# Kernel optimization log

Hardware: AMD Instinct MI355X
Metric: run time of the kernel (lower is better)

Reference implementation:

```python
import jax, jax.numpy as jnp
import numpy as np
from jax import lax

B, C, H, W = 4, 64, 240, 320
K = 15   # filter_size
R = 3    # kernel_size
EPS = 1e-5
SLOPE = 0.2  # assumed LeakyReLU slope in convbnlrelu


def _bn(x, gamma, beta, mean, var):
    # inference-mode batchnorm folded into scale/shift
    inv = gamma / jnp.sqrt(var + EPS)
    return x * inv[None, :, None, None] + (beta - mean * inv)[None, :, None, None]


def _conv(x, w, pad):
    return lax.conv_general_dilated(x, w, (1, 1), [(pad, pad), (pad, pad)],
                                    dimension_numbers=('NCHW', 'OIHW', 'NCHW'))


def setup_inputs() -> dict:
    key = jax.random.key(0)
    ks = jax.random.split(key, 12)
    f32 = jnp.float32
    return dict(
        depth=jax.random.normal(ks[0], (B, 1, H, W), f32),
        feature=jax.random.normal(ks[1], (B, C, H, W), f32),
        w1=jax.random.normal(ks[2], (C, 1, 1, 1), f32) * 0.5,
        g1=jnp.ones((C,), f32), b1=jnp.zeros((C,), f32),
        m1=jax.random.normal(ks[3], (C,), f32) * 0.1,
        v1=jax.random.uniform(ks[4], (C,), f32, 0.5, 1.5),
        ww=jax.random.normal(ks[5], (R * R, 2 * C, 3, 3), f32) * 0.05,
        gw=jnp.ones((R * R,), f32), bw=jnp.zeros((R * R,), f32),
        mw=jax.random.normal(ks[6], (R * R,), f32) * 0.1,
        vw=jax.random.uniform(ks[7], (R * R,), f32, 0.5, 1.5),
        wo=jax.random.normal(ks[8], (2 * R * R, 2 * C, 3, 3), f32) * 0.02,
        go=jnp.ones((2 * R * R,), f32), bo=jnp.zeros((2 * R * R,), f32),
        mo=jax.random.normal(ks[9], (2 * R * R,), f32) * 0.1,
        vo=jax.random.uniform(ks[10], (2 * R * R,), f32, 0.5, 1.5),
    )


def reference(depth, feature, w1, g1, b1, m1, v1, ww, gw, bw, mw, vw, wo, go, bo, mo, vo):
    # depth-guided conv + bn + leaky relu
    df = _bn(_conv(depth, w1, 0), g1, b1, m1, v1)
    df = jnp.where(df >= 0, df, SLOPE * df)
    cat = jnp.concatenate([df, feature], axis=1)           # (B, 2C, H, W)
    weight = jax.nn.sigmoid(_bn(_conv(cat, ww, 1), gw, bw, mw, vw))  # (B, R^2, H, W)
    offset = _bn(_conv(cat, wo, 1), go, bo, mo, vo)                   # (B, 2R^2, H, W)

    # DKN_Interpolate (residual=True): zero-mean the per-tap weights
    weight = weight - jnp.mean(weight, axis=1, keepdims=True)

    N = B * H * W
    off = offset.transpose(0, 2, 3, 1).reshape(N, R, R, 2)   # (..., 0)=x, (..., 1)=y
    wgt = weight.transpose(0, 2, 3, 1).reshape(N, R * R)

    # unfold depth into KxK patch per output pixel (row-major ky,kx like F.unfold)
    patches = lax.conv_general_dilated_patches(depth, (K, K), (1, 1),
                                               [(K // 2, K // 2)] * 2)  # (B, K*K, H, W)
    patches = patches.transpose(0, 2, 3, 1).reshape(N, K * K)

    vals = jnp.linspace(K // 2, K // 2 + R - 1, R).astype(depth.dtype)
    gx, gy = jnp.meshgrid(vals, vals, indexing='ij')
    grid = jnp.stack([gx, gy], axis=-1)                      # (R, R, 2)
    coord = (grid[None] + off) / K * 2.0 - 1.0               # normalized coords

    # grid_sample(align_corners=True, padding_mode='zeros') bilinear on KxK patch
    ix = (coord[..., 0] + 1.0) * 0.5 * (K - 1)               # x -> width index
    iy = (coord[..., 1] + 1.0) * 0.5 * (K - 1)               # y -> height index
    x0 = jnp.floor(ix)
    y0 = jnp.floor(iy)
    wx1 = ix - x0
    wy1 = iy - y0

    def gather(xf, yf):
        valid = (xf >= 0) & (xf <= K - 1) & (yf >= 0) & (yf <= K - 1)
        xi = jnp.clip(xf, 0, K - 1).astype(jnp.int32)
        yi = jnp.clip(yf, 0, K - 1).astype(jnp.int32)
        idx = (yi * K + xi).reshape(N, R * R)
        v = jnp.take_along_axis(patches, idx, axis=1).reshape(N, R, R)
        return jnp.where(valid, v, 0.0)

    samp = (gather(x0, y0) * (1 - wx1) * (1 - wy1)
            + gather(x0 + 1, y0) * wx1 * (1 - wy1)
            + gather(x0, y0 + 1) * (1 - wx1) * wy1
            + gather(x0 + 1, y0 + 1) * wx1 * wy1)            # (N, R, R)

    out = jnp.sum(samp.reshape(N, R * R) * wgt, axis=1).reshape(B, 1, H, W)
    return out + depth
```

## Files before the change

kernel.cpp:

```cpp
#include <hip/hip_runtime.h>
#include <hip/hip_bf16.h>
#include <math.h>

namespace {
constexpr int Bn = 4, Cn = 64, Hn = 240, Wn = 320;
constexpr int HW = Hn * Wn;
constexpr int Npix = Bn * HW;
constexpr float EPS = 1e-5f;
constexpr float SLOPE = 0.2f;
constexpr int TM = 16, TN = 16;
constexpr int HR = TM + 2, HC = TN + 2;
constexpr int NPXT = HR * HC;
constexpr int NGR = NPXT * 4;
constexpr int PHB = 1344 * 16;
constexpr int WROWS = 31, WCOLS = 31;
constexpr size_t BMAT_BYTES = 4 * 9 * 2 * 64 * 8 * 2;
constexpr size_t CONST_BYTES = 1024;
constexpr size_t PLANE_BYTES = (size_t)Bn * HW * 32 * 2;
constexpr size_t LO_OFF = BMAT_BYTES + CONST_BYTES;
constexpr size_t HI_OFF = LO_OFF + PLANE_BYTES;
constexpr size_t WS_NEED = HI_OFF + PLANE_BYTES;
}

typedef __attribute__((ext_vector_type(8))) short bf16x8;
typedef __attribute__((ext_vector_type(4))) float f32x4;

__device__ inline unsigned cvtpk(float lo, float hi) {
    unsigned r;
    asm("v_cvt_pk_bf16_f32 %0, %1, %2" : "=v"(r) : "v"(lo), "v"(hi));
    return r;
}

__device__ inline float fastexp(float x) {
    float e;
    asm("v_exp_f32 %0, %1" : "=v"(e) : "v"(x * 1.44269504f));
    return e;
}

__device__ inline float fastrcp(float x) {
    float r;
    asm("v_rcp_f32 %0, %1" : "=v"(r) : "v"(x));
    return r;
}

__device__ inline unsigned short f2bf(float f) {
    unsigned u = __builtin_bit_cast(unsigned, f);
    return (unsigned short)((u + 0x7fffu + ((u >> 16) & 1u)) >> 16);
}

__global__ __launch_bounds__(256) void prep_B(
    const float* __restrict__ ww, const float* __restrict__ wo,
    const float* __restrict__ w1, const float* __restrict__ g1,
    const float* __restrict__ b1, const float* __restrict__ m1,
    const float* __restrict__ v1,
    const float* __restrict__ gw, const float* __restrict__ bw,
    const float* __restrict__ mw, const float* __restrict__ vw,
    const float* __restrict__ go, const float* __restrict__ bo,
    const float* __restrict__ mo, const float* __restrict__ vo,
    unsigned short* __restrict__ Bf, float* __restrict__ cst)
{
    if (blockIdx.x == 18) {
        const int i = threadIdx.x;
        if (i < 64) {
            const float inv = g1[i] * rsqrtf(v1[i] + EPS);
            cst[i] = w1[i] * inv;
            cst[64 + i] = b1[i] - m1[i] * inv;
        } else if (i < 64 + 27) {
            const int j = i - 64;
            float g, bb, m, v;
            if (j < 9) { g = gw[j]; bb = bw[j]; m = mw[j]; v = vw[j]; }
            else       { g = go[j - 9]; bb = bo[j - 9]; m = mo[j - 9]; v = vo[j - 9]; }
            const float inv = g * rsqrtf(v + EPS);
            cst[128 + j] = inv;
            cst[155 + j] = bb - m * inv;
        }
        return;
    }
    const int f = blockIdx.x * 256 + threadIdx.x;
    if (f >= 4608) return;
    const int lane = f & 63, rest = f >> 6;
    const int n = rest & 1, tp = rest >> 1;
    const int t = tp % 9, p = tp / 9;
    const int col = n * 16 + (lane & 15);
    const int hi = lane >> 4;
    unsigned short o[8];
    #pragma unroll
    for (int j = 0; j < 8; ++j) {
        const int c = p * 32 + hi * 8 + j;
        float v = 0.0f;
        if (col < 9)       v = ww[((size_t)col * 128 + c) * 9 + t];
        else if (col < 27) v = wo[((size_t)(col - 9) * 128 + c) * 9 + t];
        o[j] = f2bf(v);
    }
    uint4 u;
    u.x = (unsigned)o[0] | ((unsigned)o[1] << 16);
    u.y = (unsigned)o[2] | ((unsigned)o[3] << 16);
    u.z = (unsigned)o[4] | ((unsigned)o[5] << 16);
    u.w = (unsigned)o[6] | ((unsigned)o[7] << 16);
    *(uint4*)(Bf + (size_t)f * 8) = u;
}

__global__ __launch_bounds__(512) void prep_F(
    const float* __restrict__ feature,
    unsigned short* __restrict__ lo, unsigned short* __restrict__ hi)
{
    const int y = blockIdx.x;
    const int b = blockIdx.y;
    const int lane = threadIdx.x & 63;
    const int g = threadIdx.x >> 6;
    const int c0 = g * 8;
    unsigned short* __restrict__ plane = (g < 4) ? lo : hi;
    const int slotg = g & 3;
    const float* __restrict__ fb = feature + (size_t)b * Cn * HW + (size_t)y * Wn;
    #pragma unroll
    for (int s = 0; s < 5; ++s) {
        const int x = s * 64 + lane;
        float v[8];
        #pragma unroll
        for (int j = 0; j < 8; ++j)
            v[j] = fb[(size_t)(c0 + j) * HW + x];
        uint4 u;
        u.x = cvtpk(v[0], v[1]); u.y = cvtpk(v[2], v[3]);
        u.z = cvtpk(v[4], v[5]); u.w = cvtpk(v[6], v[7]);
        const int slot = (slotg + ((x + 1) >> 1)) & 3;
        *(uint4*)(plane + (size_t)(b * HW + y * Wn + x) * 32 + slot * 8) = u;
    }
}

__global__ __launch_bounds__(256, 3) void dkn_main(
    const unsigned short* __restrict__ Bf,
    const float* __restrict__ cst,
    const unsigned short* __restrict__ catLo,
    const unsigned short* __restrict__ catHi,
    const float* __restrict__ depth,
    float* __restrict__ out)
{
    __shared__ __align__(16) char lds[2 * PHB];

    const int tid = threadIdx.x;
    const int lane = tid & 63, wv = tid >> 6;
    const int b = blockIdx.z;
    const int h0 = blockIdx.y * TM;
    const int w0 = blockIdx.x * TN;
    const float* __restrict__ dimg = depth + (size_t)b * HW;
    const float* __restrict__ dfA = cst;
    const float* __restrict__ dfB = cst + 64;
    const float* __restrict__ eInv = cst + 128;
    const float* __restrict__ eBias = cst + 155;

    char* buf0 = lds;
    char* buf1 = lds + PHB;
    float* winp = (float*)lds;
    float* ldsT = (float*)(lds + 3968);

    const bool interior = (blockIdx.y >= 1) && (blockIdx.y <= 13)
                       && (blockIdx.x >= 1) && (blockIdx.x <= 18);

    const int gdf = tid & 3;
    const int pxq = tid >> 2;
    auto stage_df = [&](int pt, char* buf) {
        const int c0 = pt * 32 + gdf * 8;
        const float4 A0 = *(const float4*)(dfA + c0);
        const float4 A1 = *(const float4*)(dfA + c0 + 4);
        const float4 B0 = *(const float4*)(dfB + c0);
        const float4 B1 = *(const float4*)(dfB + c0 + 4);
        const float Ac[8] = {A0.x, A0.y, A0.z, A0.w, A1.x, A1.y, A1.z, A1.w};
        const float Bc[8] = {B0.x, B0.y, B0.z, B0.w, B1.x, B1.y, B1.z, B1.w};
        #pragma unroll
        for (int s = 0; s < 6; ++s) {
            const int px = s * 64 + pxq;
            if (px < NPXT) {
                const int r = (px * 57) >> 10;
                const int lc = px - r * 18;
                const int y = h0 + r - 1, x = w0 + lc - 1;
                const bool ok = ((unsigned)y < (unsigned)Hn) && ((unsigned)x < (unsigned)Wn);
                const float d = ok ? dimg[y * Wn + x] : 0.0f;
                float v[8];
                #pragma unroll
                for (int j = 0; j < 8; ++j) {
                    float u = fmaf(Ac[j], d, Bc[j]);
                    u = fmaxf(u, SLOPE * u);
                    v[j] = ok ? u : 0.0f;
                }
                uint4 u4;
                u4.x = cvtpk(v[0], v[1]); u4.y = cvtpk(v[2], v[3]);
                u4.z = cvtpk(v[4], v[5]); u4.w = cvtpk(v[6], v[7]);
                const int slot = (gdf + (lc >> 1)) & 3;
                *(uint4*)(buf + px * 64 + slot * 16) = u4;
            }
        }
    };

    auto issue_gll = [&](const unsigned short* __restrict__ plane, char* buf) {
        #pragma unroll
        for (int s = 0; s < 6; ++s) {
            const int base = s * 256 + wv * 64;
            if (base < NGR) {
                int i = base + lane;
                i = min(i, NGR - 1);
                const int px = i >> 2, slot = i & 3;
                const int r = (px * 57) >> 10;
                const int lc = px - r * 18;
                const int y = min(max(h0 + r - 1, 0), Hn - 1);
                const int x = min(max(w0 + lc - 1, 0), Wn - 1);
                const unsigned short* src =
                    plane + (size_t)(b * HW + y * Wn + x) * 32 + slot * 8;
                __builtin_amdgcn_global_load_lds(
                    (const __attribute__((address_space(1))) void*)src,
                    (__attribute__((address_space(3))) void*)(buf + (size_t)base * 16),
                    16, 0, 0);
            }
        }
    };
    auto borderfix = [&](char* buf) {
        #pragma unroll
        for (int s = 0; s < 6; ++s) {
            const int i = s * 256 + tid;
            if (i < NGR) {
                const int px = i >> 2;
                const int r = (px * 57) >> 10;
                const int lc = px - r * 18;
                const int y = h0 + r - 1, x = w0 + lc - 1;
                if (((unsigned)y >= (unsigned)Hn) || ((unsigned)x >= (unsigned)Wn)) {
                    uint4 z = {0u, 0u, 0u, 0u};
                    *(uint4*)(buf + (size_t)i * 16) = z;
                }
            }
        }
    };

    const int l15 = lane & 15, hi16 = lane >> 4;
    f32x4 acc[4][2] = {};

    auto mfma_phase = [&](int p, const char* buf) {
        const unsigned short* Bp = Bf + (size_t)p * 9216;
        auto lda = [&](int row, int dx) -> bf16x8 {
            const int col = l15 + dx;
            const int slot = (hi16 + (col >> 1)) & 3;
            return *(const bf16x8*)(buf + (row * HC + col) * 64 + slot * 16);
        };
        auto ldb = [&](int idx) -> bf16x8 {
            return *(const bf16x8*)(Bp + ((size_t)idx * 64 + lane) * 8);
        };
        auto do_dy = [&](const bf16x8* A0, const bf16x8* A1,
                         const bf16x8* A2, const bf16x8* A3, const bf16x8* bb) {
            #pragma unroll
            for (int dx = 0; dx < 3; ++dx) {
                acc[0][0] = __builtin_amdgcn_mfma_f32_16x16x32_bf16(A0[dx], bb[dx*2+0], acc[0][0], 0, 0, 0);
                acc[0][1] = __builtin_amdgcn_mfma_f32_16x16x32_bf16(A0[dx], bb[dx*2+1], acc[0][1], 0, 0, 0);
                acc[1][0] = __builtin_amdgcn_mfma_f32_16x16x32_bf16(A1[dx], bb[dx*2+0], acc[1][0], 0, 0, 0);
                acc[1][1] = __builtin_amdgcn_mfma_f32_16x16x32_bf16(A1[dx], bb[dx*2+1], acc[1][1], 0, 0, 0);
                acc[2][0] = __builtin_amdgcn_mfma_f32_16x16x32_bf16(A2[dx], bb[dx*2+0], acc[2][0], 0, 0, 0);
                acc[2][1] = __builtin_amdgcn_mfma_f32_16x16x32_bf16(A2[dx], bb[dx*2+1], acc[2][1], 0, 0, 0);
                acc[3][0] = __builtin_amdgcn_mfma_f32_16x16x32_bf16(A3[dx], bb[dx*2+0], acc[3][0], 0, 0, 0);
                acc[3][1] = __builtin_amdgcn_mfma_f32_16x16x32_bf16(A3[dx], bb[dx*2+1], acc[3][1], 0, 0, 0);
            }
        };
        const int r0 = 4 * wv;
        bf16x8 a0[3], a1[3], a2[3], a3[3], a4[3], a5[3];
        bf16x8 b0[6], b1[6], b2[6];
        #pragma unroll
        for (int dx = 0; dx < 3; ++dx) {
            a0[dx] = lda(r0 + 0, dx);
            a1[dx] = lda(r0 + 1, dx);
            a2[dx] = lda(r0 + 2, dx);
            a3[dx] = lda(r0 + 3, dx);
        }
        #pragma unroll
        for (int i = 0; i < 6; ++i) b0[i] = ldb(i);
        #pragma unroll
        for (int dx = 0; dx < 3; ++dx) a4[dx] = lda(r0 + 4, dx);
        #pragma unroll
        for (int i = 0; i < 6; ++i) b1[i] = ldb(6 + i);
        do_dy(a0, a1, a2, a3, b0);
        #pragma unroll
        for (int dx = 0; dx < 3; ++dx) a5[dx] = lda(r0 + 5, dx);
        #pragma unroll
        for (int i = 0; i < 6; ++i) b2[i] = ldb(12 + i);
        do_dy(a1, a2, a3, a4, b1);
        do_dy(a2, a3, a4, a5, b2);
    };

    stage_df(0, buf0);
    __syncthreads();

    mfma_phase(0, buf0);
    stage_df(1, buf1);
    __syncthreads();

    issue_gll(catLo, buf0);
    mfma_phase(1, buf1);
    asm volatile("s_waitcnt vmcnt(0)" ::: "memory");
    if (!interior) borderfix(buf0);
    __syncthreads();

    issue_gll(catHi, buf1);
    mfma_phase(2, buf0);
    asm volatile("s_waitcnt vmcnt(0)" ::: "memory");
    if (!interior) borderfix(buf1);
    __syncthreads();

    float wvv[4];
    int widx[4];
    bool wok[4];
    #pragma unroll
    for (int s = 0; s < 4; ++s) {
        const int i = s * 256 + tid;
        const int r = (i * 2115) >> 16;
        const int c = i - r * 31;
        const int y = h0 + r - 7, x = w0 + c - 7;
        const bool inw = (i < WROWS * WCOLS);
        const bool oki = inw && ((unsigned)y < (unsigned)Hn) && ((unsigned)x < (unsigned)Wn);
        widx[s] = i;
        wok[s] = inw;
        wvv[s] = oki ? dimg[y * Wn + x] : 0.0f;
    }
    mfma_phase(3, buf1);
    #pragma unroll
    for (int s = 0; s < 4; ++s)
        if (wok[s]) winp[widx[s]] = wvv[s];
    __syncthreads();

    #pragma unroll
    for (int m = 0; m < 4; ++m) {
        const int oy = 4 * wv + m;
        #pragma unroll
        for (int n = 0; n < 2; ++n) {
            #pragma unroll
            for (int r = 0; r < 4; ++r) {
                const int ox = hi16 * 4 + r;
                ldsT[(oy * TN + ox) * 33 + n * 16 + l15] = acc[m][n][r];
            }
        }
    }
    __syncthreads();

    {
        const int oyl = tid >> 4, oxl = tid & 15;
        const int h = h0 + oyl, w = w0 + oxl;
        const float* row = ldsT + (size_t)tid * 33;

        float wgt[9];
        float wsum = 0.0f;
        #pragma unroll
        for (int j = 0; j < 9; ++j) {
            const float x = fmaf(row[j], eInv[j], eBias[j]);
            const float e = fastexp(x);
            const float s = e * fastrcp(1.0f + e);
            wgt[j] = s;
            wsum += s;
        }
        const float wm = wsum * (1.0f / 9.0f);
        #pragma unroll
        for (int j = 0; j < 9; ++j) wgt[j] -= wm;

        float offv[18];
        #pragma unroll
        for (int j = 0; j < 18; ++j)
            offv[j] = fmaf(row[9 + j], eInv[9 + j], eBias[9 + j]);

        auto sampleW = [&](float xf, float yf) -> float {
            const bool vld = (xf >= 0.0f) & (xf <= 14.0f) & (yf >= 0.0f) & (yf <= 14.0f);
            const int xi = min(max((int)xf, 0), 14);
            const int yi = min(max((int)yf, 0), 14);
            const float v = winp[(oyl + yi) * WCOLS + (oxl + xi)];
            return vld ? v : 0.0f;
        };

        float res = 0.0f;
        #pragma unroll
        for (int i = 0; i < 3; ++i) {
            #pragma unroll
            for (int j = 0; j < 3; ++j) {
                const int t = i * 3 + j;
                const float ox = offv[2 * t + 0];
                const float oy = offv[2 * t + 1];
                const float ix = (7.0f + (float)i + ox) * (14.0f / 15.0f);
                const float iy = (7.0f + (float)j + oy) * (14.0f / 15.0f);
                const float x0 = floorf(ix), y0 = floorf(iy);
                const float wx1 = ix - x0, wy1 = iy - y0;
                const float wx0 = 1.0f - wx1, wy0 = 1.0f - wy1;
                const float s =
                      sampleW(x0,        y0       ) * wx0 * wy0
                    + sampleW(x0 + 1.0f, y0       ) * wx1 * wy0
                    + sampleW(x0,        y0 + 1.0f) * wx0 * wy1
                    + sampleW(x0 + 1.0f, y0 + 1.0f) * wx1 * wy1;
                res = fmaf(s, wgt[t], res);
            }
        }
        out[((size_t)b * Hn + h) * Wn + w] = res + winp[(oyl + 7) * WCOLS + (oxl + 7)];
    }
}

__global__ __launch_bounds__(256) void dkn_fused_f32(
    const float* __restrict__ depth, const float* __restrict__ feature,
    const float* __restrict__ w1, const float* __restrict__ g1,
    const float* __restrict__ b1, const float* __restrict__ m1,
    const float* __restrict__ v1, const float* __restrict__ ww,
    const float* __restrict__ gw, const float* __restrict__ bw,
    const float* __restrict__ mw, const float* __restrict__ vw,
    const float* __restrict__ wo, const float* __restrict__ go,
    const float* __restrict__ bo, const float* __restrict__ mo,
    const float* __restrict__ vo, float* __restrict__ out)
{
    const int n = blockIdx.x * blockDim.x + threadIdx.x;
    if (n >= Npix) return;
    const int w = n % Wn;
    const int h = (n / Wn) % Hn;
    const int b = n / (Wn * Hn);
    const float* __restrict__ dimg = depth + (size_t)b * HW;
    const float* __restrict__ fimg = feature + (size_t)b * Cn * HW;
    float d9[9], msk[9]; int off9[9];
    #pragma unroll
    for (int ky = 0; ky < 3; ++ky)
        #pragma unroll
        for (int kx = 0; kx < 3; ++kx) {
            const int t = ky * 3 + kx;
            const int y = h + ky - 1, x = w + kx - 1;
            const bool ok = ((unsigned)y < (unsigned)Hn) && ((unsigned)x < (unsigned)Wn);
            off9[t] = min(max(y, 0), Hn - 1) * Wn + min(max(x, 0), Wn - 1);
            d9[t] = dimg[off9[t]];
            msk[t] = ok ? 1.0f : 0.0f;
        }
    float accW[9], accO[18];
    #pragma unroll
    for (int o = 0; o < 9; ++o) accW[o] = 0.0f;
    #pragma unroll
    for (int o = 0; o < 18; ++o) accO[o] = 0.0f;
    for (int c = 0; c < Cn; ++c) {
        const float inv = g1[c] * rsqrtf(v1[c] + EPS);
        const float A = w1[c] * inv, Bc = b1[c] - m1[c] * inv;
        float v9[9];
        #pragma unroll
        for (int t = 0; t < 9; ++t) {
            const float x = fmaf(A, d9[t], Bc);
            v9[t] = msk[t] * fmaxf(x, SLOPE * x);
        }
        const float* wwc = ww + c * 9;
        const float* woc = wo + c * 9;
        #pragma unroll
        for (int o = 0; o < 9; ++o)
            #pragma unroll
            for (int t = 0; t < 9; ++t) accW[o] = fmaf(wwc[o * 1152 + t], v9[t], accW[o]);
        #pragma unroll
        for (int o = 0; o < 18; ++o)
            #pragma unroll
            for (int t = 0; t < 9; ++t) accO[o] = fmaf(woc[o * 1152 + t], v9[t], accO[o]);
    }
    for (int c = 0; c < Cn; ++c) {
        const float* fc = fimg + (size_t)c * HW;
        float v9[9];
        #pragma unroll
        for (int t = 0; t < 9; ++t) v9[t] = msk[t] * fc[off9[t]];
        const float* wwc = ww + (64 + c) * 9;
        const float* woc = wo + (64 + c) * 9;
        #pragma unroll
        for (int o = 0; o < 9; ++o)
            #pragma unroll
            for (int t = 0; t < 9; ++t) accW[o] = fmaf(wwc[o * 1152 + t], v9[t], accW[o]);
        #pragma unroll
        for (int o = 0; o < 18; ++o)
            #pragma unroll
            for (int t = 0; t < 9; ++t) accO[o] = fmaf(woc[o * 1152 + t], v9[t], accO[o]);
    }
    float wgt[9];
    float wsum = 0.0f;
    #pragma unroll
    for (int j = 0; j < 9; ++j) {
        const float inv = gw[j] * rsqrtf(vw[j] + EPS);
        const float x = fmaf(accW[j], inv, bw[j] - mw[j] * inv);
        const float s = 1.0f / (1.0f + expf(-x));
        wgt[j] = s; wsum += s;
    }
    const float wm = wsum * (1.0f / 9.0f);
    #pragma unroll
    for (int j = 0; j < 9; ++j) wgt[j] -= wm;
    float offv[18];
    #pragma unroll
    for (int j = 0; j < 18; ++j) {
        const float inv = go[j] * rsqrtf(vo[j] + EPS);
        offv[j] = fmaf(accO[j], inv, bo[j] - mo[j] * inv);
    }
    auto sampleD = [&](float xf, float yf) -> float {
        const bool vld = (xf >= 0.0f) & (xf <= 14.0f) & (yf >= 0.0f) & (yf <= 14.0f);
        const float xc = fminf(fmaxf(xf, 0.0f), 14.0f);
        const float yc = fminf(fmaxf(yf, 0.0f), 14.0f);
        const int xi = (int)xc, yi = (int)yc;
        const int yy = h + yi - 7, xx = w + xi - 7;
        const bool okimg = ((unsigned)yy < (unsigned)Hn) && ((unsigned)xx < (unsigned)Wn);
        return (vld && okimg) ? dimg[yy * Wn + xx] : 0.0f;
    };
    float res = 0.0f;
    #pragma unroll
    for (int i = 0; i < 3; ++i)
        #pragma unroll
        for (int j = 0; j < 3; ++j) {
            const int t = i * 3 + j;
            const float ox = offv[2 * t + 0], oy = offv[2 * t + 1];
            const float ix = (7.0f + (float)i + ox) * (14.0f / 15.0f);
            const float iy = (7.0f + (float)j + oy) * (14.0f / 15.0f);
            const float x0 = floorf(ix), y0 = floorf(iy);
            const float wx1 = ix - x0, wy1 = iy - y0;
            const float s = sampleD(x0, y0) * (1.0f - wx1) * (1.0f - wy1)
                          + sampleD(x0 + 1.0f, y0) * wx1 * (1.0f - wy1)
                          + sampleD(x0, y0 + 1.0f) * (1.0f - wx1) * wy1
                          + sampleD(x0 + 1.0f, y0 + 1.0f) * wx1 * wy1;
            res = fmaf(s, wgt[t], res);
        }
    out[n] = res + dimg[h * Wn + w];
}

extern "C" void kernel_launch(void* const* d_in, const int* in_sizes, int n_in,
                              void* d_out, int out_size, void* d_ws, size_t ws_size,
                              hipStream_t stream) {
    (void)in_sizes; (void)n_in; (void)out_size;
    const float* depth   = (const float*)d_in[0];
    const float* feature = (const float*)d_in[1];
    const float* w1 = (const float*)d_in[2];
    const float* g1 = (const float*)d_in[3];
    const float* b1 = (const float*)d_in[4];
    const float* m1 = (const float*)d_in[5];
    const float* v1 = (const float*)d_in[6];
    const float* ww = (const float*)d_in[7];
    const float* gw = (const float*)d_in[8];
    const float* bw = (const float*)d_in[9];
    const float* mw = (const float*)d_in[10];
    const float* vw = (const float*)d_in[11];
    const float* wo = (const float*)d_in[12];
    const float* go = (const float*)d_in[13];
    const float* bo = (const float*)d_in[14];
    const float* mo = (const float*)d_in[15];
    const float* vo = (const float*)d_in[16];
    float* out = (float*)d_out;

    if (ws_size >= WS_NEED) {
        unsigned short* Bmat  = (unsigned short*)d_ws;
        float* cst = (float*)((char*)d_ws + BMAT_BYTES);
        unsigned short* catLo = (unsigned short*)((char*)d_ws + LO_OFF);
        unsigned short* catHi = (unsigned short*)((char*)d_ws + HI_OFF);
        hipLaunchKernelGGL(prep_B, dim3(19), dim3(256), 0, stream,
                           ww, wo, w1, g1, b1, m1, v1,
                           gw, bw, mw, vw, go, bo, mo, vo, Bmat, cst);
        hipLaunchKernelGGL(prep_F, dim3(Hn, Bn), dim3(512), 0, stream,
                           feature, catLo, catHi);
        hipLaunchKernelGGL(dkn_main, dim3(Wn / TN, Hn / TM, Bn), dim3(256), 0, stream,
                           Bmat, cst, catLo, catHi, depth, out);
    } else {
        hipLaunchKernelGGL(dkn_fused_f32, dim3((Npix + 255) / 256), dim3(256), 0, stream,
                           depth, feature, w1, g1, b1, m1, v1,
                           ww, gw, bw, mw, vw, wo, go, bo, mo, vo, out);
    }
}
```

Measured before the change: 66.89 us.

## Build depth-feature MFMA operands in registers and prefetch both feature planes upfront

The depth-derived half of the concatenated input (conv1x1+BN+LeakyReLU) is now computed directly in registers per lane from cached depth values, so it no longer goes through LDS staging and its barriers. Both bf16 feature-plane loads are issued into LDS at kernel start, overlapping with the register-only depth-channel MFMA phases. Phases then run with only one barrier before the feature MFMAs. This cuts LDS traffic and sync points but adds redundant per-lane conversion ALU work, more registers, and a larger LDS footprint (separate window buffer), which may reduce occupancy.

```diff
diff --git a/kernel.cpp b/kernel.cpp
--- a/kernel.cpp
+++ b/kernel.cpp
@@ -135,10 +135,11 @@
     const float* __restrict__ depth,
     float* __restrict__ out)
 {
-    __shared__ __align__(16) char lds[2 * PHB];
+    __shared__ __align__(16) char lds[2 * PHB + 3968];
 
     const int tid = threadIdx.x;
     const int lane = tid & 63, wv = tid >> 6;
+    const int l15 = lane & 15, hi16 = lane >> 4;
     const int b = blockIdx.z;
     const int h0 = blockIdx.y * TM;
     const int w0 = blockIdx.x * TN;
@@ -150,46 +151,56 @@
 
     char* buf0 = lds;
     char* buf1 = lds + PHB;
-    float* winp = (float*)lds;
-    float* ldsT = (float*)(lds + 3968);
+    float* winp = (float*)(lds + 2 * PHB);
+    float* ldsT = (float*)lds;
 
     const bool interior = (blockIdx.y >= 1) && (blockIdx.y <= 13)
                        && (blockIdx.x >= 1) && (blockIdx.x <= 18);
 
-    const int gdf = tid & 3;
-    const int pxq = tid >> 2;
-    auto stage_df = [&](int pt, char* buf) {
-        const int c0 = pt * 32 + gdf * 8;
-        const float4 A0 = *(const float4*)(dfA + c0);
-        const float4 A1 = *(const float4*)(dfA + c0 + 4);
-        const float4 B0 = *(const float4*)(dfB + c0);
-        const float4 B1 = *(const float4*)(dfB + c0 + 4);
-        const float Ac[8] = {A0.x, A0.y, A0.z, A0.w, A1.x, A1.y, A1.z, A1.w};
-        const float Bc[8] = {B0.x, B0.y, B0.z, B0.w, B1.x, B1.y, B1.z, B1.w};
-        #pragma unroll
-        for (int s = 0; s < 6; ++s) {
-            const int px = s * 64 + pxq;
-            if (px < NPXT) {
-                const int r = (px * 57) >> 10;
-                const int lc = px - r * 18;
-                const int y = h0 + r - 1, x = w0 + lc - 1;
-                const bool ok = ((unsigned)y < (unsigned)Hn) && ((unsigned)x < (unsigned)Wn);
-                const float d = ok ? dimg[y * Wn + x] : 0.0f;
-                float v[8];
-                #pragma unroll
-                for (int j = 0; j < 8; ++j) {
-                    float u = fmaf(Ac[j], d, Bc[j]);
-                    u = fmaxf(u, SLOPE * u);
-                    v[j] = ok ? u : 0.0f;
-                }
-                uint4 u4;
-                u4.x = cvtpk(v[0], v[1]); u4.y = cvtpk(v[2], v[3]);
-                u4.z = cvtpk(v[4], v[5]); u4.w = cvtpk(v[6], v[7]);
-                const int slot = (gdf + (lc >> 1)) & 3;
-                *(uint4*)(buf + px * 64 + slot * 16) = u4;
-            }
-        }
-    };
+    float wvv[4];
+    int widx[4];
+    bool wok[4];
+    #pragma unroll
+    for (int s = 0; s < 4; ++s) {
+        const int i = s * 256 + tid;
+        const int r = (i * 2115) >> 16;
+        const int c = i - r * 31;
+        const int y = h0 + r - 7, x = w0 + c - 7;
+        const bool inw = (i < WROWS * WCOLS);
+        const bool oki = inw && ((unsigned)y < (unsigned)Hn) && ((unsigned)x < (unsigned)Wn);
+        widx[s] = i;
+        wok[s] = inw;
+        wvv[s] = oki ? dimg[y * Wn + x] : 0.0f;
+    }
+
+    const int r0 = 4 * wv;
+    float dreg[6][3], oky6[6], okx3[3];
+    #pragma unroll
+    for (int dx = 0; dx < 3; ++dx) {
+        const int x = w0 + l15 + dx - 1;
+        okx3[dx] = ((unsigned)x < (unsigned)Wn) ? 1.0f : 0.0f;
+    }
+    #pragma unroll
+    for (int i = 0; i < 6; ++i) {
+        const int y = h0 + r0 + i - 1;
+        oky6[i] = ((unsigned)y < (unsigned)Hn) ? 1.0f : 0.0f;
+        const int yc = min(max(y, 0), Hn - 1);
+        #pragma unroll
+        for (int dx = 0; dx < 3; ++dx) {
+            const int x = w0 + l15 + dx - 1;
+            const int xc = min(max(x, 0), Wn - 1);
+            dreg[i][dx] = dimg[yc * Wn + xc];
+        }
+    }
+
+    float A8[2][8], B8[2][8];
+    #pragma unroll
+    for (int p = 0; p < 2; ++p)
+        #pragma unroll
+        for (int j = 0; j < 8; ++j) {
+            A8[p][j] = dfA[p * 32 + hi16 * 8 + j];
+            B8[p][j] = dfB[p * 32 + hi16 * 8 + j];
+        }
 
     auto issue_gll = [&](const unsigned short* __restrict__ plane, char* buf) {
         #pragma unroll
@@ -212,6 +223,9 @@
             }
         }
     };
+    issue_gll(catLo, buf0);
+    issue_gll(catHi, buf1);
+
     auto borderfix = [&](char* buf) {
         #pragma unroll
         for (int s = 0; s < 6; ++s) {
@@ -229,10 +243,66 @@
         }
     };
 
-    const int l15 = lane & 15, hi16 = lane >> 4;
     f32x4 acc[4][2] = {};
 
-    auto mfma_phase = [&](int p, const char* buf) {
+    auto do_dy = [&](const bf16x8* Aq0, const bf16x8* Aq1,
+                     const bf16x8* Aq2, const bf16x8* Aq3, const bf16x8* bb) {
+        #pragma unroll
+        for (int dx = 0; dx < 3; ++dx) {
+            acc[0][0] = __builtin_amdgcn_mfma_f32_16x16x32_bf16(Aq0[dx], bb[dx*2+0], acc[0][0], 0, 0, 0);
+            acc[0][1] = __builtin_amdgcn_mfma_f32_16x16x32_bf16(Aq0[dx], bb[dx*2+1], acc[0][1], 0, 0, 0);
+            acc[1][0] = __builtin_amdgcn_mfma_f32_16x16x32_bf16(Aq1[dx], bb[dx*2+0], acc[1][0], 0, 0, 0);
+            acc[1][1] = __builtin_amdgcn_mfma_f32_16x16x32_bf16(Aq1[dx], bb[dx*2+1], acc[1][1], 0, 0, 0);
+            acc[2][0] = __builtin_amdgcn_mfma_f32_16x16x32_bf16(Aq2[dx], bb[dx*2+0], acc[2][0], 0, 0, 0);
+            acc[2][1] = __builtin_amdgcn_mfma_f32_16x16x32_bf16(Aq2[dx], bb[dx*2+1], acc[2][1], 0, 0, 0);
+            acc[3][0] = __builtin_amdgcn_mfma_f32_16x16x32_bf16(Aq3[dx], bb[dx*2+0], acc[3][0], 0, 0, 0);
+            acc[3][1] = __builtin_amdgcn_mfma_f32_16x16x32_bf16(Aq3[dx], bb[dx*2+1], acc[3][1], 0, 0, 0);
+        }
+    };
+
+    auto mfma_df = [&](int p) {
+        const unsigned short* Bp = Bf + (size_t)p * 9216;
+        auto ldb = [&](int idx) -> bf16x8 {
+            return *(const bf16x8*)(Bp + ((size_t)idx * 64 + lane) * 8);
+        };
+        auto mk = [&](int i, int dx) -> bf16x8 {
+            const float dd = dreg[i][dx];
+            const float okf = oky6[i] * okx3[dx];
+            float vv[8];
+            #pragma unroll
+            for (int j = 0; j < 8; ++j) {
+                float u = fmaf(A8[p][j], dd, B8[p][j]);
+                u = fmaxf(u, SLOPE * u);
+                vv[j] = u * okf;
+            }
+            union { uint4 q; bf16x8 v; } r;
+            r.q.x = cvtpk(vv[0], vv[1]); r.q.y = cvtpk(vv[2], vv[3]);
+            r.q.z = cvtpk(vv[4], vv[5]); r.q.w = cvtpk(vv[6], vv[7]);
+            return r.v;
+        };
+        bf16x8 a0[3], a1[3], a2[3], a3[3], a4[3], a5[3];
+        bf16x8 b0[6], b1[6], b2[6];
+        #pragma unroll
+        for (int dx = 0; dx < 3; ++dx) {
+            a0[dx] = mk(0, dx); a1[dx] = mk(1, dx);
+            a2[dx] = mk(2, dx); a3[dx] = mk(3, dx);
+        }
+        #pragma unroll
+        for (int i = 0; i < 6; ++i) b0[i] = ldb(i);
+        #pragma unroll
+        for (int dx = 0; dx < 3; ++dx) a4[dx] = mk(4, dx);
+        #pragma unroll
+        for (int i = 0; i < 6; ++i) b1[i] = ldb(6 + i);
+        do_dy(a0, a1, a2, a3, b0);
+        #pragma unroll
+        for (int dx = 0; dx < 3; ++dx) a5[dx] = mk(5, dx);
+        #pragma unroll
+        for (int i = 0; i < 6; ++i) b2[i] = ldb(12 + i);
+        do_dy(a1, a2, a3, a4, b1);
+        do_dy(a2, a3, a4, a5, b2);
+    };
+
+    auto mfma_feat = [&](int p, const char* buf) {
         const unsigned short* Bp = Bf + (size_t)p * 9216;
         auto lda = [&](int row, int dx) -> bf16x8 {
             const int col = l15 + dx;
@@ -242,29 +312,12 @@
         auto ldb = [&](int idx) -> bf16x8 {
             return *(const bf16x8*)(Bp + ((size_t)idx * 64 + lane) * 8);
         };
-        auto do_dy = [&](const bf16x8* A0, const bf16x8* A1,
-                         const bf16x8* A2, const bf16x8* A3, const bf16x8* bb) {
-            #pragma unroll
-            for (int dx = 0; dx < 3; ++dx) {
-                acc[0][0] = __builtin_amdgcn_mfma_f32_16x16x32_bf16(A0[dx], bb[dx*2+0], acc[0][0], 0, 0, 0);
-                acc[0][1] = __builtin_amdgcn_mfma_f32_16x16x32_bf16(A0[dx], bb[dx*2+1], acc[0][1], 0, 0, 0);
-                acc[1][0] = __builtin_amdgcn_mfma_f32_16x16x32_bf16(A1[dx], bb[dx*2+0], acc[1][0], 0, 0, 0);
-                acc[1][1] = __builtin_amdgcn_mfma_f32_16x16x32_bf16(A1[dx], bb[dx*2+1], acc[1][1], 0, 0, 0);
-                acc[2][0] = __builtin_amdgcn_mfma_f32_16x16x32_bf16(A2[dx], bb[dx*2+0], acc[2][0], 0, 0, 0);
-                acc[2][1] = __builtin_amdgcn_mfma_f32_16x16x32_bf16(A2[dx], bb[dx*2+1], acc[2][1], 0, 0, 0);
-                acc[3][0] = __builtin_amdgcn_mfma_f32_16x16x32_bf16(A3[dx], bb[dx*2+0], acc[3][0], 0, 0, 0);
-                acc[3][1] = __builtin_amdgcn_mfma_f32_16x16x32_bf16(A3[dx], bb[dx*2+1], acc[3][1], 0, 0, 0);
-            }
-        };
-        const int r0 = 4 * wv;
         bf16x8 a0[3], a1[3], a2[3], a3[3], a4[3], a5[3];
         bf16x8 b0[6], b1[6], b2[6];
         #pragma unroll
         for (int dx = 0; dx < 3; ++dx) {
-            a0[dx] = lda(r0 + 0, dx);
-            a1[dx] = lda(r0 + 1, dx);
-            a2[dx] = lda(r0 + 2, dx);
-            a3[dx] = lda(r0 + 3, dx);
+            a0[dx] = lda(r0 + 0, dx); a1[dx] = lda(r0 + 1, dx);
+            a2[dx] = lda(r0 + 2, dx); a3[dx] = lda(r0 + 3, dx);
         }
         #pragma unroll
         for (int i = 0; i < 6; ++i) b0[i] = ldb(i);
@@ -281,44 +334,18 @@
         do_dy(a2, a3, a4, a5, b2);
     };
 
-    stage_df(0, buf0);
-    __syncthreads();
-
-    mfma_phase(0, buf0);
-    stage_df(1, buf1);
-    __syncthreads();
-
-    issue_gll(catLo, buf0);
-    mfma_phase(1, buf1);
+    mfma_df(0);
+    mfma_df(1);
+
     asm volatile("s_waitcnt vmcnt(0)" ::: "memory");
-    if (!interior) borderfix(buf0);
-    __syncthreads();
-
-    issue_gll(catHi, buf1);
-    mfma_phase(2, buf0);
-    asm volatile("s_waitcnt vmcnt(0)" ::: "memory");
-    if (!interior) borderfix(buf1);
-    __syncthreads();
-
-    float wvv[4];
-    int widx[4];
-    bool wok[4];
-    #pragma unroll
-    for (int s = 0; s < 4; ++s) {
-        const int i = s * 256 + tid;
-        const int r = (i * 2115) >> 16;
-        const int c = i - r * 31;
-        const int y = h0 + r - 7, x = w0 + c - 7;
-        const bool inw = (i < WROWS * WCOLS);
-        const bool oki = inw && ((unsigned)y < (unsigned)Hn) && ((unsigned)x < (unsigned)Wn);
-        widx[s] = i;
-        wok[s] = inw;
-        wvv[s] = oki ? dimg[y * Wn + x] : 0.0f;
-    }
-    mfma_phase(3, buf1);
     #pragma unroll
     for (int s = 0; s < 4; ++s)
         if (wok[s]) winp[widx[s]] = wvv[s];
+    if (!interior) { borderfix(buf0); borderfix(buf1); }
+    __syncthreads();
+
+    mfma_feat(2, buf0);
+    mfma_feat(3, buf1);
     __syncthreads();
 
     #pragma unroll
```

Result: slower. 76.61 us (+14.5%).

## Single-buffer main kernel LDS for higher occupancy and merge prep kernels

Applied to the files above, without the earlier changes.

Merges the weight-prep and feature-prep kernels into one launch by adding an extra grid row for the weight and constant work. In the main kernel, the double-buffered LDS staging becomes a single buffer with a separate depth-window region, and launch bounds rise from 3 to 5 blocks per CU. The transposed accumulator store shrinks its stride from 33 to 27 floats and skips unused columns. The cost is extra barriers and the loss of overlap between global loads, depth staging and MFMA phases, which are now serialized.

```diff
diff --git a/kernel.cpp b/kernel.cpp
--- a/kernel.cpp
+++ b/kernel.cpp
@@ -14,6 +14,8 @@
 constexpr int NGR = NPXT * 4;
 constexpr int PHB = 1344 * 16;
 constexpr int WROWS = 31, WCOLS = 31;
+constexpr int WINP_OFF = 27648;
+constexpr int LDS_TOTAL = WINP_OFF + 3968;
 constexpr size_t BMAT_BYTES = 4 * 9 * 2 * 64 * 8 * 2;
 constexpr size_t CONST_BYTES = 1024;
 constexpr size_t PLANE_BYTES = (size_t)Bn * HW * 32 * 2;
@@ -48,7 +50,8 @@
     return (unsigned short)((u + 0x7fffu + ((u >> 16) & 1u)) >> 16);
 }
 
-__global__ __launch_bounds__(256) void prep_B(
+__global__ __launch_bounds__(512) void prep_FB(
+    const float* __restrict__ feature,
     const float* __restrict__ ww, const float* __restrict__ wo,
     const float* __restrict__ w1, const float* __restrict__ g1,
     const float* __restrict__ b1, const float* __restrict__ m1,
@@ -57,57 +60,55 @@
     const float* __restrict__ mw, const float* __restrict__ vw,
     const float* __restrict__ go, const float* __restrict__ bo,
     const float* __restrict__ mo, const float* __restrict__ vo,
+    unsigned short* __restrict__ lo, unsigned short* __restrict__ hi,
     unsigned short* __restrict__ Bf, float* __restrict__ cst)
 {
-    if (blockIdx.x == 18) {
-        const int i = threadIdx.x;
-        if (i < 64) {
-            const float inv = g1[i] * rsqrtf(v1[i] + EPS);
-            cst[i] = w1[i] * inv;
-            cst[64 + i] = b1[i] - m1[i] * inv;
-        } else if (i < 64 + 27) {
-            const int j = i - 64;
-            float g, bb, m, v;
-            if (j < 9) { g = gw[j]; bb = bw[j]; m = mw[j]; v = vw[j]; }
-            else       { g = go[j - 9]; bb = bo[j - 9]; m = mo[j - 9]; v = vo[j - 9]; }
-            const float inv = g * rsqrtf(v + EPS);
-            cst[128 + j] = inv;
-            cst[155 + j] = bb - m * inv;
+    const int tid = threadIdx.x;
+    if (blockIdx.y == Bn) {
+        const int bx = blockIdx.x;
+        if (bx < 9) {
+            const int f = bx * 512 + tid;
+            const int lane = f & 63, rest = f >> 6;
+            const int n = rest & 1, tp = rest >> 1;
+            const int t = tp % 9, p = tp / 9;
+            const int col = n * 16 + (lane & 15);
+            const int hh = lane >> 4;
+            unsigned short o[8];
+            #pragma unroll
+            for (int j = 0; j < 8; ++j) {
+                const int c = p * 32 + hh * 8 + j;
+                float v = 0.0f;
+                if (col < 9)       v = ww[((size_t)col * 128 + c) * 9 + t];
+                else if (col < 27) v = wo[((size_t)(col - 9) * 128 + c) * 9 + t];
+                o[j] = f2bf(v);
+            }
+            uint4 u;
+            u.x = (unsigned)o[0] | ((unsigned)o[1] << 16);
+            u.y = (unsigned)o[2] | ((unsigned)o[3] << 16);
+            u.z = (unsigned)o[4] | ((unsigned)o[5] << 16);
+            u.w = (unsigned)o[6] | ((unsigned)o[7] << 16);
+            *(uint4*)(Bf + (size_t)f * 8) = u;
+        } else if (bx == 9) {
+            if (tid < 64) {
+                const float inv = g1[tid] * rsqrtf(v1[tid] + EPS);
+                cst[tid] = w1[tid] * inv;
+                cst[64 + tid] = b1[tid] - m1[tid] * inv;
+            } else if (tid < 64 + 27) {
+                const int j = tid - 64;
+                float g, bb, m, v;
+                if (j < 9) { g = gw[j]; bb = bw[j]; m = mw[j]; v = vw[j]; }
+                else       { g = go[j - 9]; bb = bo[j - 9]; m = mo[j - 9]; v = vo[j - 9]; }
+                const float inv = g * rsqrtf(v + EPS);
+                cst[128 + j] = inv;
+                cst[155 + j] = bb - m * inv;
+            }
         }
         return;
     }
-    const int f = blockIdx.x * 256 + threadIdx.x;
-    if (f >= 4608) return;
-    const int lane = f & 63, rest = f >> 6;
-    const int n = rest & 1, tp = rest >> 1;
-    const int t = tp % 9, p = tp / 9;
-    const int col = n * 16 + (lane & 15);
-    const int hi = lane >> 4;
-    unsigned short o[8];
-    #pragma unroll
-    for (int j = 0; j < 8; ++j) {
-        const int c = p * 32 + hi * 8 + j;
-        float v = 0.0f;
-        if (col < 9)       v = ww[((size_t)col * 128 + c) * 9 + t];
-        else if (col < 27) v = wo[((size_t)(col - 9) * 128 + c) * 9 + t];
-        o[j] = f2bf(v);
-    }
-    uint4 u;
-    u.x = (unsigned)o[0] | ((unsigned)o[1] << 16);
-    u.y = (unsigned)o[2] | ((unsigned)o[3] << 16);
-    u.z = (unsigned)o[4] | ((unsigned)o[5] << 16);
-    u.w = (unsigned)o[6] | ((unsigned)o[7] << 16);
-    *(uint4*)(Bf + (size_t)f * 8) = u;
-}
-
-__global__ __launch_bounds__(512) void prep_F(
-    const float* __restrict__ feature,
-    unsigned short* __restrict__ lo, unsigned short* __restrict__ hi)
-{
     const int y = blockIdx.x;
     const int b = blockIdx.y;
-    const int lane = threadIdx.x & 63;
-    const int g = threadIdx.x >> 6;
+    const int lane = tid & 63;
+    const int g = tid >> 6;
     const int c0 = g * 8;
     unsigned short* __restrict__ plane = (g < 4) ? lo : hi;
     const int slotg = g & 3;
@@ -127,7 +128,7 @@
     }
 }
 
-__global__ __launch_bounds__(256, 3) void dkn_main(
+__global__ __launch_bounds__(256, 5) void dkn_main(
     const unsigned short* __restrict__ Bf,
     const float* __restrict__ cst,
     const unsigned short* __restrict__ catLo,
@@ -135,10 +136,11 @@
     const float* __restrict__ depth,
     float* __restrict__ out)
 {
-    __shared__ __align__(16) char lds[2 * PHB];
+    __shared__ __align__(16) char lds[LDS_TOTAL];
 
     const int tid = threadIdx.x;
     const int lane = tid & 63, wv = tid >> 6;
+    const int l15 = lane & 15, hi16 = lane >> 4;
     const int b = blockIdx.z;
     const int h0 = blockIdx.y * TM;
     const int w0 = blockIdx.x * TN;
@@ -148,17 +150,28 @@
     const float* __restrict__ eInv = cst + 128;
     const float* __restrict__ eBias = cst + 155;
 
-    char* buf0 = lds;
-    char* buf1 = lds + PHB;
-    float* winp = (float*)lds;
-    float* ldsT = (float*)(lds + 3968);
+    char* S = lds;
+    float* winp = (float*)(lds + WINP_OFF);
+    float* ldsT = (float*)lds;
 
     const bool interior = (blockIdx.y >= 1) && (blockIdx.y <= 13)
                        && (blockIdx.x >= 1) && (blockIdx.x <= 18);
 
+    #pragma unroll
+    for (int s = 0; s < 4; ++s) {
+        const int i = s * 256 + tid;
+        const int r = (i * 2115) >> 16;
+        const int c = i - r * 31;
+        const int y = h0 + r - 7, x = w0 + c - 7;
+        const bool inw = (i < WROWS * WCOLS);
+        const bool oki = inw && ((unsigned)y < (unsigned)Hn) && ((unsigned)x < (unsigned)Wn);
+        const float v = oki ? dimg[y * Wn + x] : 0.0f;
+        if (inw) winp[i] = v;
+    }
+
     const int gdf = tid & 3;
     const int pxq = tid >> 2;
-    auto stage_df = [&](int pt, char* buf) {
+    auto stage_df = [&](int pt) {
         const int c0 = pt * 32 + gdf * 8;
         const float4 A0 = *(const float4*)(dfA + c0);
         const float4 A1 = *(const float4*)(dfA + c0 + 4);
@@ -186,12 +199,12 @@
                 u4.x = cvtpk(v[0], v[1]); u4.y = cvtpk(v[2], v[3]);
                 u4.z = cvtpk(v[4], v[5]); u4.w = cvtpk(v[6], v[7]);
                 const int slot = (gdf + (lc >> 1)) & 3;
-                *(uint4*)(buf + px * 64 + slot * 16) = u4;
+                *(uint4*)(S + px * 64 + slot * 16) = u4;
             }
         }
     };
 
-    auto issue_gll = [&](const unsigned short* __restrict__ plane, char* buf) {
+    auto issue_gll = [&](const unsigned short* __restrict__ plane) {
         #pragma unroll
         for (int s = 0; s < 6; ++s) {
             const int base = s * 256 + wv * 64;
@@ -207,12 +220,12 @@
                     plane + (size_t)(b * HW + y * Wn + x) * 32 + slot * 8;
                 __builtin_amdgcn_global_load_lds(
                     (const __attribute__((address_space(1))) void*)src,
-                    (__attribute__((address_space(3))) void*)(buf + (size_t)base * 16),
+                    (__attribute__((address_space(3))) void*)(S + (size_t)base * 16),
                     16, 0, 0);
             }
         }
     };
-    auto borderfix = [&](char* buf) {
+    auto borderfix = [&]() {
         #pragma unroll
         for (int s = 0; s < 6; ++s) {
             const int i = s * 256 + tid;
@@ -223,21 +236,21 @@
                 const int y = h0 + r - 1, x = w0 + lc - 1;
                 if (((unsigned)y >= (unsigned)Hn) || ((unsigned)x >= (unsigned)Wn)) {
                     uint4 z = {0u, 0u, 0u, 0u};
-                    *(uint4*)(buf + (size_t)i * 16) = z;
+                    *(uint4*)(S + (size_t)i * 16) = z;
                 }
             }
         }
     };
 
-    const int l15 = lane & 15, hi16 = lane >> 4;
     f32x4 acc[4][2] = {};
-
-    auto mfma_phase = [&](int p, const char* buf) {
+    const int r0 = 4 * wv;
+
+    auto mfma_phase = [&](int p) {
         const unsigned short* Bp = Bf + (size_t)p * 9216;
         auto lda = [&](int row, int dx) -> bf16x8 {
             const int col = l15 + dx;
             const int slot = (hi16 + (col >> 1)) & 3;
-            return *(const bf16x8*)(buf + (row * HC + col) * 64 + slot * 16);
+            return *(const bf16x8*)(S + (row * HC + col) * 64 + slot * 16);
         };
         auto ldb = [&](int idx) -> bf16x8 {
             return *(const bf16x8*)(Bp + ((size_t)idx * 64 + lane) * 8);
@@ -256,15 +269,12 @@
                 acc[3][1] = __builtin_amdgcn_mfma_f32_16x16x32_bf16(A3[dx], bb[dx*2+1], acc[3][1], 0, 0, 0);
             }
         };
-        const int r0 = 4 * wv;
         bf16x8 a0[3], a1[3], a2[3], a3[3], a4[3], a5[3];
         bf16x8 b0[6], b1[6], b2[6];
         #pragma unroll
         for (int dx = 0; dx < 3; ++dx) {
-            a0[dx] = lda(r0 + 0, dx);
-            a1[dx] = lda(r0 + 1, dx);
-            a2[dx] = lda(r0 + 2, dx);
-            a3[dx] = lda(r0 + 3, dx);
+            a0[dx] = lda(r0 + 0, dx); a1[dx] = lda(r0 + 1, dx);
+            a2[dx] = lda(r0 + 2, dx); a3[dx] = lda(r0 + 3, dx);
         }
         #pragma unroll
         for (int i = 0; i < 6; ++i) b0[i] = ldb(i);
@@ -281,44 +291,28 @@
         do_dy(a2, a3, a4, a5, b2);
     };
 
-    stage_df(0, buf0);
-    __syncthreads();
-
-    mfma_phase(0, buf0);
-    stage_df(1, buf1);
-    __syncthreads();
-
-    issue_gll(catLo, buf0);
-    mfma_phase(1, buf1);
+    stage_df(0);
+    __syncthreads();
+    mfma_phase(0);
+    __syncthreads();
+
+    stage_df(1);
+    __syncthreads();
+    mfma_phase(1);
+    __syncthreads();
+
+    issue_gll(catLo);
     asm volatile("s_waitcnt vmcnt(0)" ::: "memory");
-    if (!interior) borderfix(buf0);
-    __syncthreads();
-
-    issue_gll(catHi, buf1);
-    mfma_phase(2, buf0);
+    if (!interior) borderfix();
+    __syncthreads();
+    mfma_phase(2);
+    __syncthreads();
+
+    issue_gll(catHi);
     asm volatile("s_waitcnt vmcnt(0)" ::: "memory");
-    if (!interior) borderfix(buf1);
-    __syncthreads();
-
-    float wvv[4];
-    int widx[4];
-    bool wok[4];
-    #pragma unroll
-    for (int s = 0; s < 4; ++s) {
-        const int i = s * 256 + tid;
-        const int r = (i * 2115) >> 16;
-        const int c = i - r * 31;
-        const int y = h0 + r - 7, x = w0 + c - 7;
-        const bool inw = (i < WROWS * WCOLS);
-        const bool oki = inw && ((unsigned)y < (unsigned)Hn) && ((unsigned)x < (unsigned)Wn);
-        widx[s] = i;
-        wok[s] = inw;
-        wvv[s] = oki ? dimg[y * Wn + x] : 0.0f;
-    }
-    mfma_phase(3, buf1);
-    #pragma unroll
-    for (int s = 0; s < 4; ++s)
-        if (wok[s]) winp[widx[s]] = wvv[s];
+    if (!interior) borderfix();
+    __syncthreads();
+    mfma_phase(3);
     __syncthreads();
 
     #pragma unroll
@@ -326,10 +320,12 @@
         const int oy = 4 * wv + m;
         #pragma unroll
         for (int n = 0; n < 2; ++n) {
-            #pragma unroll
-            for (int r = 0; r < 4; ++r) {
-                const int ox = hi16 * 4 + r;
-                ldsT[(oy * TN + ox) * 33 + n * 16 + l15] = acc[m][n][r];
+            if (n == 0 || l15 < 11) {
+                #pragma unroll
+                for (int r = 0; r < 4; ++r) {
+                    const int ox = hi16 * 4 + r;
+                    ldsT[(oy * TN + ox) * 27 + n * 16 + l15] = acc[m][n][r];
+                }
             }
         }
     }
@@ -338,7 +334,7 @@
     {
         const int oyl = tid >> 4, oxl = tid & 15;
         const int h = h0 + oyl, w = w0 + oxl;
-        const float* row = ldsT + (size_t)tid * 33;
+        const float* row = ldsT + (size_t)tid * 27;
 
         float wgt[9];
         float wsum = 0.0f;
@@ -538,11 +534,10 @@
         float* cst = (float*)((char*)d_ws + BMAT_BYTES);
         unsigned short* catLo = (unsigned short*)((char*)d_ws + LO_OFF);
         unsigned short* catHi = (unsigned short*)((char*)d_ws + HI_OFF);
-        hipLaunchKernelGGL(prep_B, dim3(19), dim3(256), 0, stream,
-                           ww, wo, w1, g1, b1, m1, v1,
-                           gw, bw, mw, vw, go, bo, mo, vo, Bmat, cst);
-        hipLaunchKernelGGL(prep_F, dim3(Hn, Bn), dim3(512), 0, stream,
-                           feature, catLo, catHi);
+        hipLaunchKernelGGL(prep_FB, dim3(Hn, Bn + 1), dim3(512), 0, stream,
+                           feature, ww, wo, w1, g1, b1, m1, v1,
+                           gw, bw, mw, vw, go, bo, mo, vo,
+                           catLo, catHi, Bmat, cst);
         hipLaunchKernelGGL(dkn_main, dim3(Wn / TN, Hn / TM, Bn), dim3(256), 0, stream,
                            Bmat, cst, catLo, catHi, depth, out);
     } else {
```

Measured after the change: 72.79 us. 8.8% more time.
